# Kernel tuning notes

Measured on AMD Instinct MI355X. Metric: run time of the kernel, lower is better.

The kernel has to match this reference:

```python
import jax, jax.numpy as jnp
import numpy as np

B, S, H, E, TOP_K = 4, 2048, 1024, 8, 2


def setup_inputs() -> dict:
    key = jax.random.key(0)
    ks = jax.random.split(key, 7)
    sc = 1.0 / np.sqrt(H)
    return {
        "x": jax.random.normal(ks[0], (B, S, H), dtype=jnp.float32),
        "gate_w": jax.random.normal(ks[1], (H, E), dtype=jnp.float32) * sc,
        "gate_b": jnp.zeros((E,), dtype=jnp.float32),
        "w1": jax.random.normal(ks[2], (E, H, H), dtype=jnp.float32) * sc,
        "b1": jnp.zeros((E, H), dtype=jnp.float32),
        "w2": jax.random.normal(ks[3], (E, H, H), dtype=jnp.float32) * sc,
        "b2": jnp.zeros((E, H), dtype=jnp.float32),
    }


def reference(x, gate_w, gate_b, w1, b1, w2, b2):
    b, s, h = x.shape
    e = gate_w.shape[1]
    t = b * s
    hs = x.reshape(t, h)                                   # [T,H] flattened tokens
    # --- Router ---
    router_logits = hs @ gate_w + gate_b                    # [T,E] (returned pre-softmax)
    probs = jax.nn.softmax(router_logits, axis=-1)
    top_v, top_i = jax.lax.top_k(probs, TOP_K)              # [T,K]
    router_weight = top_v / top_v.sum(axis=-1, keepdims=True)
    # Dense per-(token, expert) gate: 0 for unselected experts -> same math as
    # the torch gather/index_add_ dispatch-combine loop.
    gates = jnp.zeros((t, e), hs.dtype).at[
        jnp.arange(t)[:, None], top_i
    ].add(router_weight)                                    # [T,E]
    # --- Experts (BasicExpert: Linear -> ReLU -> Linear, H->H->H) ---
    h1 = jax.nn.relu(jnp.einsum("th,ehf->etf", hs, w1) + b1[:, None, :])  # [E,T,H]
    oe = jnp.einsum("etf,efg->etg", h1, w2) + b2[:, None, :]              # [E,T,H]
    out = jnp.einsum("etg,te->tg", oe, gates)               # weighted combine [T,H]
    return out.reshape(b, s, h), router_logits
```

## Files before the change

### kernel.cpp

```cpp
#include <hip/hip_runtime.h>
#include <hip/hip_bf16.h>

#define T_TOKENS 8192
#define H_DIM    1024
#define N_EXP    8

#define BM 64
#define BN 128
#define BK 64

#define MAX_MSLOT 264
#define GEMM_GRID (MAX_MSLOT * 8)

typedef __attribute__((ext_vector_type(8))) __bf16 bf16x8;
typedef __attribute__((ext_vector_type(4))) float  f32x4;

#define AS1(p) ((const __attribute__((address_space(1))) void*)(p))
#define AS3(p) ((__attribute__((address_space(3))) void*)(p))

__device__ __forceinline__ unsigned short f2bf(float f) {
  unsigned u = __float_as_uint(f);
  u += 0x7fff + ((u >> 16) & 1);
  return (unsigned short)(u >> 16);
}
__device__ __forceinline__ float bf2f(unsigned short s) {
  return __uint_as_float(((unsigned)s) << 16);
}

__global__ __launch_bounds__(256) void router_kernel(
    const float* __restrict__ x, const float* __restrict__ gw,
    const float* __restrict__ gb, float* __restrict__ logits_out,
    int* __restrict__ choice, float* __restrict__ wpair,
    unsigned short* __restrict__ xb)
{
  const int tid = threadIdx.x;
  const int lane = tid & 63;
  const int w = tid >> 6;
  const int t = blockIdx.x * 4 + w;
  const float* xr = x + (size_t)t * H_DIM;

  float acc[8];
  #pragma unroll
  for (int e = 0; e < 8; ++e) acc[e] = 0.f;

  #pragma unroll
  for (int i = 0; i < H_DIM / 64; ++i) {
    const int h = i * 64 + lane;
    const float xv = xr[h];
    if (xb) xb[(size_t)t * H_DIM + h] = f2bf(xv);
    const float4 g0 = *(const float4*)&gw[h * 8 + 0];
    const float4 g1 = *(const float4*)&gw[h * 8 + 4];
    acc[0] += xv * g0.x; acc[1] += xv * g0.y;
    acc[2] += xv * g0.z; acc[3] += xv * g0.w;
    acc[4] += xv * g1.x; acc[5] += xv * g1.y;
    acc[6] += xv * g1.z; acc[7] += xv * g1.w;
  }
  #pragma unroll
  for (int off = 32; off; off >>= 1) {
    #pragma unroll
    for (int e = 0; e < 8; ++e) acc[e] += __shfl_xor(acc[e], off);
  }
  if (lane == 0) {
    float lg[8];
    #pragma unroll
    for (int e = 0; e < 8; ++e) lg[e] = acc[e] + gb[e];
    #pragma unroll
    for (int e = 0; e < 8; ++e) logits_out[(size_t)t * N_EXP + e] = lg[e];
    int e0 = 0; float v0 = lg[0];
    #pragma unroll
    for (int e = 1; e < 8; ++e) { if (lg[e] > v0) { v0 = lg[e]; e0 = e; } }
    int e1 = -1; float v1 = -3.4e38f;
    #pragma unroll
    for (int e = 0; e < 8; ++e) { if (e != e0 && lg[e] > v1) { v1 = lg[e]; e1 = e; } }
    const float ew = expf(v1 - v0);
    const float r0 = 1.f / (1.f + ew);
    const float r1 = ew / (1.f + ew);
    wpair[2 * t + 0] = r0;
    wpair[2 * t + 1] = r1;
    choice[t] = e0 | (e1 << 4);
  }
}

__global__ __launch_bounds__(256) void build_lists_kernel(
    const int* __restrict__ choice, int* __restrict__ cnt, int* __restrict__ lst)
{
  const int e = blockIdx.x;
  const int tid = threadIdx.x;
  __shared__ int sc[256];

  const int t0 = tid * 32;
  int ch[32];
  int cl = 0;
  #pragma unroll
  for (int j = 0; j < 32; ++j) {
    ch[j] = choice[t0 + j];
    if ((ch[j] & 15) == e) cl++;
    if ((ch[j] >> 4) == e) cl++;
  }
  sc[tid] = cl;
  __syncthreads();
  #pragma unroll
  for (int off = 1; off < 256; off <<= 1) {
    int u = (tid >= off) ? sc[tid - off] : 0;
    __syncthreads();
    sc[tid] += u;
    __syncthreads();
  }
  int pos = sc[tid] - cl;
  int* le = lst + e * T_TOKENS;
  #pragma unroll
  for (int j = 0; j < 32; ++j) {
    if ((ch[j] & 15) == e) le[pos++] = 2 * (t0 + j);
    if ((ch[j] >> 4) == e) le[pos++] = 2 * (t0 + j) + 1;
  }
  if (tid == 255) cnt[e] = sc[255];
}

__global__ void sched_kernel(const int* __restrict__ cnt, int* __restrict__ msched)
{
  if (threadIdx.x == 0) {
    int s = 0;
    for (int e = 0; e < N_EXP; ++e) {
      const int nm = (cnt[e] + BM - 1) / BM;
      for (int i = 0; i < nm; ++i) msched[s++] = e | (i << 4);
    }
    for (; s < MAX_MSLOT; ++s) msched[s] = -1;
  }
}

__global__ __launch_bounds__(256) void wconv_kernel(
    const float* __restrict__ w, unsigned short* __restrict__ wt)
{
  __shared__ float t[64][65];
  const float* we = w + (size_t)blockIdx.z * H_DIM * H_DIM;
  unsigned short* wte = wt + (size_t)blockIdx.z * H_DIM * H_DIM;
  const int k0 = blockIdx.y * 64, n0 = blockIdx.x * 64;
  const int tid = threadIdx.x;
  #pragma unroll
  for (int r = 0; r < 4; ++r) {
    const int k = (tid >> 4) + r * 16;
    const int n = (tid & 15) * 4;
    const float4 v = *(const float4*)&we[(size_t)(k0 + k) * H_DIM + n0 + n];
    t[n + 0][k] = v.x; t[n + 1][k] = v.y; t[n + 2][k] = v.z; t[n + 3][k] = v.w;
  }
  __syncthreads();
  const int n = tid >> 2, kc = (tid & 3) * 16;
  unsigned short o[16];
  #pragma unroll
  for (int j = 0; j < 16; ++j) o[j] = f2bf(t[n][kc + j]);
  *(int4*)&wte[(size_t)(n0 + n) * H_DIM + k0 + kc] = *(int4*)&o[0];
  *(int4*)&wte[(size_t)(n0 + n) * H_DIM + k0 + kc + 8] = *(int4*)&o[8];
}

#define DECODE_SLOT()                                        \
  const int id = blockIdx.x;                                 \
  const int sv = msched[(id >> 6) * 8 + (id & 7)];           \
  if (sv < 0) return;                                        \
  const int e  = sv & 15;                                    \
  const int m0 = (sv >> 4) * BM;                             \
  const int n0 = ((id >> 3) & 7) * BN;

template<int XB>
__global__ __launch_bounds__(256, 4) void gemm1_kernel(
    const float* __restrict__ x, const unsigned short* __restrict__ xb,
    const unsigned short* __restrict__ w1t, const float* __restrict__ b1,
    const int* __restrict__ cnt, const int* __restrict__ lst,
    const int* __restrict__ msched,
    const float* __restrict__ wpair, unsigned short* __restrict__ h1)
{
  DECODE_SLOT();
  const int c = cnt[e];
  const unsigned short* W = w1t + (size_t)e * H_DIM * H_DIM;
  const int* le = lst + e * T_TOKENS;

  __shared__ unsigned short As[BM * BK];
  __shared__ unsigned short Bs[BN * BK];

  const int tid  = threadIdx.x;
  const int lane = tid & 63;
  const int wid  = tid >> 6;

  const int lrow8 = lane >> 3;
  const int csrc  = (lane & 7) ^ lrow8;

  const unsigned short* bSrc[4];
  #pragma unroll
  for (int i = 0; i < 4; ++i) {
    const int r = wid * 32 + i * 8 + lrow8;
    bSrc[i] = W + (size_t)(n0 + r) * H_DIM + csrc * 8;
  }

  const unsigned short* aSrcB[2];
  const float* aSrcF[4]; int adst[4];
  if constexpr (XB) {
    #pragma unroll
    for (int i = 0; i < 2; ++i) {
      const int m = wid * 16 + i * 8 + lrow8;
      const int gm = m0 + m;
      const int pair = (gm < c) ? le[gm] : le[0];
      aSrcB[i] = xb + (size_t)(pair >> 1) * H_DIM + csrc * 8;
    }
  } else {
    #pragma unroll
    for (int i = 0; i < 4; ++i) {
      const int idx = i * 256 + tid;
      const int m = idx >> 4;
      const int k4 = (idx & 15) << 2;
      const int gm = m0 + m;
      const int pair = (gm < c) ? le[gm] : le[0];
      aSrcF[i] = x + (size_t)(pair >> 1) * H_DIM + k4;
      adst[i] = m * BK + (k4 ^ ((m & 7) << 3));
    }
  }

  const int wr = (wid >> 1) * 32;
  const int wc = (wid & 1) * 64;
  const int lr = lane & 15;
  const int kh = (lane >> 4) << 3;
  const int sw = (lane & 7) << 3;

  f32x4 acc[2][4];
  #pragma unroll
  for (int i = 0; i < 2; ++i)
    #pragma unroll
    for (int j = 0; j < 4; ++j) acc[i][j] = (f32x4){0.f, 0.f, 0.f, 0.f};

  for (int kt = 0; kt < H_DIM; kt += BK) {
    __syncthreads();
    #pragma unroll
    for (int i = 0; i < 4; ++i)
      __builtin_amdgcn_global_load_lds(AS1(bSrc[i] + kt), AS3(&Bs[(wid * 32 + i * 8) * BK]), 16, 0, 0);
    if constexpr (XB) {
      #pragma unroll
      for (int i = 0; i < 2; ++i)
        __builtin_amdgcn_global_load_lds(AS1(aSrcB[i] + kt), AS3(&As[(wid * 16 + i * 8) * BK]), 16, 0, 0);
    } else {
      #pragma unroll
      for (int i = 0; i < 4; ++i) {
        const float4 v = *(const float4*)(aSrcF[i] + kt);
        short4 s4;
        ((unsigned short*)&s4)[0] = f2bf(v.x);
        ((unsigned short*)&s4)[1] = f2bf(v.y);
        ((unsigned short*)&s4)[2] = f2bf(v.z);
        ((unsigned short*)&s4)[3] = f2bf(v.w);
        *(short4*)&As[adst[i]] = s4;
      }
    }
    __syncthreads();
    #pragma unroll
    for (int kk = 0; kk < BK; kk += 32) {
      bf16x8 a[2], b[4];
      #pragma unroll
      for (int mi = 0; mi < 2; ++mi) {
        const int row = wr + mi * 16 + lr;
        a[mi] = *reinterpret_cast<const bf16x8*>(&As[row * BK + ((kk + kh) ^ sw)]);
      }
      #pragma unroll
      for (int ni = 0; ni < 4; ++ni) {
        const int row = wc + ni * 16 + lr;
        b[ni] = *reinterpret_cast<const bf16x8*>(&Bs[row * BK + ((kk + kh) ^ sw)]);
      }
      #pragma unroll
      for (int mi = 0; mi < 2; ++mi)
        #pragma unroll
        for (int ni = 0; ni < 4; ++ni)
          acc[mi][ni] = __builtin_amdgcn_mfma_f32_16x16x32_bf16(a[mi], b[ni], acc[mi][ni], 0, 0, 0);
    }
  }

  #pragma unroll
  for (int mi = 0; mi < 2; ++mi) {
    const int rbase = wr + mi * 16 + ((lane >> 4) << 2);
    #pragma unroll
    for (int r = 0; r < 4; ++r) {
      const int gm = m0 + rbase + r;
      if (gm >= c) continue;
      const int pair = le[gm];
      const float g = wpair[pair];
      unsigned short* dst = h1 + (size_t)pair * H_DIM;
      #pragma unroll
      for (int ni = 0; ni < 4; ++ni) {
        const int col = n0 + wc + ni * 16 + lr;
        const float v = acc[mi][ni][r] + b1[e * H_DIM + col];
        dst[col] = f2bf(g * fmaxf(v, 0.f));
      }
    }
  }
}

__global__ __launch_bounds__(256, 4) void gemm2_kernel(
    const unsigned short* __restrict__ h1, const unsigned short* __restrict__ w2t,
    const float* __restrict__ b2, const int* __restrict__ cnt,
    const int* __restrict__ lst, const int* __restrict__ msched,
    const float* __restrict__ wpair,
    unsigned short* __restrict__ oe, float* __restrict__ out)
{
  DECODE_SLOT();
  const int c = cnt[e];
  const unsigned short* W = w2t + (size_t)e * H_DIM * H_DIM;
  const int* le = lst + e * T_TOKENS;

  __shared__ unsigned short As[BM * BK];
  __shared__ unsigned short Bs[BN * BK];

  const int tid  = threadIdx.x;
  const int lane = tid & 63;
  const int wid  = tid >> 6;

  const int lrow8 = lane >> 3;
  const int csrc  = (lane & 7) ^ lrow8;

  const unsigned short* aSrc[2];
  const unsigned short* bSrc[4];
  #pragma unroll
  for (int i = 0; i < 4; ++i) {
    const int r = wid * 32 + i * 8 + lrow8;
    bSrc[i] = W + (size_t)(n0 + r) * H_DIM + csrc * 8;
  }
  #pragma unroll
  for (int i = 0; i < 2; ++i) {
    const int m = wid * 16 + i * 8 + lrow8;
    const int gm = m0 + m;
    const int pair = (gm < c) ? le[gm] : le[0];
    aSrc[i] = h1 + (size_t)pair * H_DIM + csrc * 8;
  }

  const int wr = (wid >> 1) * 32;
  const int wc = (wid & 1) * 64;
  const int lr = lane & 15;
  const int kh = (lane >> 4) << 3;
  const int sw = (lane & 7) << 3;

  f32x4 acc[2][4];
  #pragma unroll
  for (int i = 0; i < 2; ++i)
    #pragma unroll
    for (int j = 0; j < 4; ++j) acc[i][j] = (f32x4){0.f, 0.f, 0.f, 0.f};

  for (int kt = 0; kt < H_DIM; kt += BK) {
    __syncthreads();
    #pragma unroll
    for (int i = 0; i < 4; ++i)
      __builtin_amdgcn_global_load_lds(AS1(bSrc[i] + kt), AS3(&Bs[(wid * 32 + i * 8) * BK]), 16, 0, 0);
    #pragma unroll
    for (int i = 0; i < 2; ++i)
      __builtin_amdgcn_global_load_lds(AS1(aSrc[i] + kt), AS3(&As[(wid * 16 + i * 8) * BK]), 16, 0, 0);
    __syncthreads();
    #pragma unroll
    for (int kk = 0; kk < BK; kk += 32) {
      bf16x8 a[2], b[4];
      #pragma unroll
      for (int mi = 0; mi < 2; ++mi) {
        const int row = wr + mi * 16 + lr;
        a[mi] = *reinterpret_cast<const bf16x8*>(&As[row * BK + ((kk + kh) ^ sw)]);
      }
      #pragma unroll
      for (int ni = 0; ni < 4; ++ni) {
        const int row = wc + ni * 16 + lr;
        b[ni] = *reinterpret_cast<const bf16x8*>(&Bs[row * BK + ((kk + kh) ^ sw)]);
      }
      #pragma unroll
      for (int mi = 0; mi < 2; ++mi)
        #pragma unroll
        for (int ni = 0; ni < 4; ++ni)
          acc[mi][ni] = __builtin_amdgcn_mfma_f32_16x16x32_bf16(a[mi], b[ni], acc[mi][ni], 0, 0, 0);
    }
  }

  #pragma unroll
  for (int mi = 0; mi < 2; ++mi) {
    const int rbase = wr + mi * 16 + ((lane >> 4) << 2);
    #pragma unroll
    for (int r = 0; r < 4; ++r) {
      const int gm = m0 + rbase + r;
      if (gm >= c) continue;
      const int pair = le[gm];
      unsigned short* dst = oe + (size_t)pair * H_DIM;
      #pragma unroll
      for (int ni = 0; ni < 4; ++ni) {
        const int col = n0 + wc + ni * 16 + lr;
        dst[col] = f2bf(acc[mi][ni][r]);
      }
    }
  }
}

__global__ __launch_bounds__(256, 4) void gemm2_atomic_kernel(
    const unsigned short* __restrict__ h1, const unsigned short* __restrict__ w2t,
    const float* __restrict__ b2, const int* __restrict__ cnt,
    const int* __restrict__ lst, const int* __restrict__ msched,
    const float* __restrict__ wpair, float* __restrict__ out)
{
  DECODE_SLOT();
  const int c = cnt[e];
  const unsigned short* W = w2t + (size_t)e * H_DIM * H_DIM;
  const int* le = lst + e * T_TOKENS;

  __shared__ unsigned short As[BM * BK];
  __shared__ unsigned short Bs[BN * BK];

  const int tid  = threadIdx.x;
  const int lane = tid & 63;
  const int wid  = tid >> 6;
  const int lrow8 = lane >> 3;
  const int csrc  = (lane & 7) ^ lrow8;

  const unsigned short* aSrc[2];
  const unsigned short* bSrc[4];
  #pragma unroll
  for (int i = 0; i < 4; ++i) {
    const int r = wid * 32 + i * 8 + lrow8;
    bSrc[i] = W + (size_t)(n0 + r) * H_DIM + csrc * 8;
  }
  #pragma unroll
  for (int i = 0; i < 2; ++i) {
    const int m = wid * 16 + i * 8 + lrow8;
    const int gm = m0 + m;
    const int pair = (gm < c) ? le[gm] : le[0];
    aSrc[i] = h1 + (size_t)pair * H_DIM + csrc * 8;
  }

  const int wr = (wid >> 1) * 32;
  const int wc = (wid & 1) * 64;
  const int lr = lane & 15;
  const int kh = (lane >> 4) << 3;
  const int sw = (lane & 7) << 3;

  f32x4 acc[2][4];
  #pragma unroll
  for (int i = 0; i < 2; ++i)
    #pragma unroll
    for (int j = 0; j < 4; ++j) acc[i][j] = (f32x4){0.f, 0.f, 0.f, 0.f};

  for (int kt = 0; kt < H_DIM; kt += BK) {
    __syncthreads();
    #pragma unroll
    for (int i = 0; i < 4; ++i)
      __builtin_amdgcn_global_load_lds(AS1(bSrc[i] + kt), AS3(&Bs[(wid * 32 + i * 8) * BK]), 16, 0, 0);
    #pragma unroll
    for (int i = 0; i < 2; ++i)
      __builtin_amdgcn_global_load_lds(AS1(aSrc[i] + kt), AS3(&As[(wid * 16 + i * 8) * BK]), 16, 0, 0);
    __syncthreads();
    #pragma unroll
    for (int kk = 0; kk < BK; kk += 32) {
      bf16x8 a[2], b[4];
      #pragma unroll
      for (int mi = 0; mi < 2; ++mi)
        a[mi] = *reinterpret_cast<const bf16x8*>(&As[(wr + mi * 16 + lr) * BK + ((kk + kh) ^ sw)]);
      #pragma unroll
      for (int ni = 0; ni < 4; ++ni)
        b[ni] = *reinterpret_cast<const bf16x8*>(&Bs[(wc + ni * 16 + lr) * BK + ((kk + kh) ^ sw)]);
      #pragma unroll
      for (int mi = 0; mi < 2; ++mi)
        #pragma unroll
        for (int ni = 0; ni < 4; ++ni)
          acc[mi][ni] = __builtin_amdgcn_mfma_f32_16x16x32_bf16(a[mi], b[ni], acc[mi][ni], 0, 0, 0);
    }
  }

  #pragma unroll
  for (int mi = 0; mi < 2; ++mi) {
    const int rbase = wr + mi * 16 + ((lane >> 4) << 2);
    #pragma unroll
    for (int r = 0; r < 4; ++r) {
      const int gm = m0 + rbase + r;
      if (gm >= c) continue;
      const int pair = le[gm];
      const int tok = pair >> 1;
      const float g = wpair[pair];
      float* dst = out + (size_t)tok * H_DIM;
      #pragma unroll
      for (int ni = 0; ni < 4; ++ni) {
        const int col = n0 + wc + ni * 16 + lr;
        atomicAdd(&dst[col], acc[mi][ni][r] + g * b2[e * H_DIM + col]);
      }
    }
  }
}

__global__ __launch_bounds__(256) void combine_kernel(
    const unsigned short* __restrict__ oe, const int* __restrict__ choice,
    const float* __restrict__ wpair, const float* __restrict__ b2,
    float* __restrict__ out)
{
  const int tid = threadIdx.x;
  const int t = blockIdx.x * 2 + (tid >> 7);
  const int col = (tid & 127) * 8;
  const int ch = choice[t];
  const int e0 = ch & 15, e1 = ch >> 4;
  const float g0 = wpair[2 * t], g1 = wpair[2 * t + 1];

  const unsigned short* o0 = oe + (size_t)(2 * t) * H_DIM + col;
  const unsigned short* o1 = oe + (size_t)(2 * t + 1) * H_DIM + col;
  int4 a = *(const int4*)o0;
  int4 b = *(const int4*)o1;
  const unsigned short* pa = (const unsigned short*)&a;
  const unsigned short* pb = (const unsigned short*)&b;
  const float* b2r0 = b2 + e0 * H_DIM + col;
  const float* b2r1 = b2 + e1 * H_DIM + col;
  float4 c0 = *(const float4*)&b2r0[0];
  float4 c1 = *(const float4*)&b2r0[4];
  float4 d0 = *(const float4*)&b2r1[0];
  float4 d1 = *(const float4*)&b2r1[4];
  float r[8];
  r[0] = bf2f(pa[0]) + bf2f(pb[0]) + g0 * c0.x + g1 * d0.x;
  r[1] = bf2f(pa[1]) + bf2f(pb[1]) + g0 * c0.y + g1 * d0.y;
  r[2] = bf2f(pa[2]) + bf2f(pb[2]) + g0 * c0.z + g1 * d0.z;
  r[3] = bf2f(pa[3]) + bf2f(pb[3]) + g0 * c0.w + g1 * d0.w;
  r[4] = bf2f(pa[4]) + bf2f(pb[4]) + g0 * c1.x + g1 * d1.x;
  r[5] = bf2f(pa[5]) + bf2f(pb[5]) + g0 * c1.y + g1 * d1.y;
  r[6] = bf2f(pa[6]) + bf2f(pb[6]) + g0 * c1.z + g1 * d1.z;
  r[7] = bf2f(pa[7]) + bf2f(pb[7]) + g0 * c1.w + g1 * d1.w;
  float* dst = out + (size_t)t * H_DIM + col;
  *(float4*)&dst[0] = *(float4*)&r[0];
  *(float4*)&dst[4] = *(float4*)&r[4];
}

extern "C" void kernel_launch(void* const* d_in, const int* in_sizes, int n_in,
                              void* d_out, int out_size, void* d_ws, size_t ws_size,
                              hipStream_t stream) {
  const float* x      = (const float*)d_in[0];
  const float* gate_w = (const float*)d_in[1];
  const float* gate_b = (const float*)d_in[2];
  const float* w1     = (const float*)d_in[3];
  const float* b1     = (const float*)d_in[4];
  const float* w2     = (const float*)d_in[5];
  const float* b2     = (const float*)d_in[6];

  float* out    = (float*)d_out;
  float* logits = out + (size_t)T_TOKENS * H_DIM;

  char* ws = (char*)d_ws;
  int*   cnt    = (int*)ws;
  int*   lst    = (int*)(ws + 256);
  float* wpr    = (float*)(ws + 262400);
  int*   choice = (int*)(ws + 327936);
  int*   msched = (int*)(ws + 360704);
  char*  big    = ws + 362752;

  const size_t SZ_XB = (size_t)T_TOKENS * H_DIM * 2;
  const size_t SZ_WT = (size_t)N_EXP * H_DIM * H_DIM * 2;
  const size_t SZ_H1 = (size_t)2 * T_TOKENS * H_DIM * 2;
  const size_t SZ_OE = (size_t)2 * T_TOKENS * H_DIM * 2;
  const bool full = ws_size >= (size_t)362752 + SZ_XB + SZ_WT + SZ_H1 + SZ_OE;

  unsigned short* xb = (unsigned short*)big;
  unsigned short* wt = (unsigned short*)(big + (full ? SZ_XB : 0));
  unsigned short* h1 = (unsigned short*)(big + (full ? SZ_XB : 0) + SZ_WT);
  unsigned short* oe = (unsigned short*)(big + SZ_XB + SZ_WT + SZ_H1);

  if (full) {
    router_kernel<<<T_TOKENS / 4, 256, 0, stream>>>(x, gate_w, gate_b, logits, choice, wpr, xb);
    build_lists_kernel<<<N_EXP, 256, 0, stream>>>(choice, cnt, lst);
    sched_kernel<<<1, 64, 0, stream>>>(cnt, msched);
    wconv_kernel<<<dim3(16, 16, 8), 256, 0, stream>>>(w1, wt);
    gemm1_kernel<1><<<GEMM_GRID, 256, 0, stream>>>(x, xb, wt, b1, cnt, lst, msched, wpr, h1);
    wconv_kernel<<<dim3(16, 16, 8), 256, 0, stream>>>(w2, wt);
    gemm2_kernel<<<GEMM_GRID, 256, 0, stream>>>(h1, wt, b2, cnt, lst, msched, wpr, oe, out);
    combine_kernel<<<T_TOKENS / 2, 256, 0, stream>>>(oe, choice, wpr, b2, out);
  } else {
    hipMemsetAsync(out, 0, (size_t)T_TOKENS * H_DIM * sizeof(float), stream);
    router_kernel<<<T_TOKENS / 4, 256, 0, stream>>>(x, gate_w, gate_b, logits, choice, wpr, nullptr);
    build_lists_kernel<<<N_EXP, 256, 0, stream>>>(choice, cnt, lst);
    sched_kernel<<<1, 64, 0, stream>>>(cnt, msched);
    wconv_kernel<<<dim3(16, 16, 8), 256, 0, stream>>>(w1, wt);
    gemm1_kernel<0><<<GEMM_GRID, 256, 0, stream>>>(x, xb, wt, b1, cnt, lst, msched, wpr, h1);
    wconv_kernel<<<dim3(16, 16, 8), 256, 0, stream>>>(w2, wt);
    gemm2_atomic_kernel<<<GEMM_GRID, 256, 0, stream>>>(h1, wt, b2, cnt, lst, msched, wpr, out);
  }
}
```

Before: 171.8 us.

## Replace grouped expert GEMMs with double-buffered 256x256-tile persistent kernel

```diff
diff --git a/kernel.cpp b/kernel.cpp
--- a/kernel.cpp
+++ b/kernel.cpp
@@ -122,7 +122,7 @@
     int s = 0;
     for (int e = 0; e < N_EXP; ++e) {
       const int nm = (cnt[e] + BM - 1) / BM;
-      for (int i = 0; i < nm; ++i) msched[s++] = e | (i << 4);
+      for (int i = 0; i < nm && s < MAX_MSLOT; ++i) msched[s++] = e | (i << 4);
     }
     for (; s < MAX_MSLOT; ++s) msched[s] = -1;
   }
@@ -150,6 +150,125 @@
   for (int j = 0; j < 16; ++j) o[j] = f2bf(t[n][kc + j]);
   *(int4*)&wte[(size_t)(n0 + n) * H_DIM + k0 + kc] = *(int4*)&o[0];
   *(int4*)&wte[(size_t)(n0 + n) * H_DIM + k0 + kc + 8] = *(int4*)&o[8];
+}
+
+template<int G1>
+__global__ __launch_bounds__(512, 2) void gemm256_kernel(
+    const unsigned short* __restrict__ A,
+    const unsigned short* __restrict__ Wt,
+    const float* __restrict__ b1,
+    const int* __restrict__ cnt, const int* __restrict__ lst,
+    const float* __restrict__ wpair,
+    unsigned short* __restrict__ Out)
+{
+  const int e   = blockIdx.x & 7;
+  const int g   = blockIdx.x >> 3;
+  const int mi  = g & 7;
+  const int n0g = (g >> 3) * 256;
+  const int c = cnt[e];
+  const unsigned short* W = Wt + (size_t)e * H_DIM * H_DIM;
+  const int* le = lst + e * T_TOKENS;
+
+  __shared__ unsigned short As[2][256 * 64];
+  __shared__ unsigned short Bs[2][256 * 64];
+
+  const int tid  = threadIdx.x;
+  const int lane = tid & 63;
+  const int wid  = tid >> 6;
+  const int wm   = wid >> 2;
+  const int wn   = wid & 3;
+  const int lrow8 = lane >> 3;
+  const int csrc  = (lane & 7) ^ lrow8;
+  const int lr = lane & 15;
+  const int kh = (lane >> 4) << 3;
+  const int sw = (lane & 7) << 3;
+
+  const unsigned short* bSrc[4];
+  #pragma unroll
+  for (int i = 0; i < 4; ++i)
+    bSrc[i] = W + (size_t)(n0g + wid * 32 + i * 8 + lrow8) * H_DIM + csrc * 8;
+
+  for (int m0 = mi * 256; m0 < c; m0 += 2048) {
+    const unsigned short* aSrc[4];
+    #pragma unroll
+    for (int i = 0; i < 4; ++i) {
+      const int gm = m0 + wid * 32 + i * 8 + lrow8;
+      const int pair = (gm < c) ? le[gm] : le[0];
+      const size_t row = G1 ? (size_t)(pair >> 1) : (size_t)pair;
+      aSrc[i] = A + row * H_DIM + csrc * 8;
+    }
+
+    f32x4 acc[8][4];
+    #pragma unroll
+    for (int i = 0; i < 8; ++i)
+      #pragma unroll
+      for (int j = 0; j < 4; ++j) acc[i][j] = (f32x4){0.f, 0.f, 0.f, 0.f};
+
+    #pragma unroll
+    for (int i = 0; i < 4; ++i) {
+      __builtin_amdgcn_global_load_lds(AS1(aSrc[i]), AS3(&As[0][(wid * 32 + i * 8) * 64]), 16, 0, 0);
+      __builtin_amdgcn_global_load_lds(AS1(bSrc[i]), AS3(&Bs[0][(wid * 32 + i * 8) * 64]), 16, 0, 0);
+    }
+
+    for (int t = 0; t < 16; ++t) {
+      __syncthreads();
+      const int cb = t & 1;
+      if (t < 15) {
+        const int kt = (t + 1) * BK;
+        #pragma unroll
+        for (int i = 0; i < 4; ++i) {
+          __builtin_amdgcn_global_load_lds(AS1(aSrc[i] + kt), AS3(&As[cb ^ 1][(wid * 32 + i * 8) * 64]), 16, 0, 0);
+          __builtin_amdgcn_global_load_lds(AS1(bSrc[i] + kt), AS3(&Bs[cb ^ 1][(wid * 32 + i * 8) * 64]), 16, 0, 0);
+        }
+      }
+      #pragma unroll
+      for (int ks = 0; ks < 2; ++ks) {
+        bf16x8 b[4];
+        #pragma unroll
+        for (int nf = 0; nf < 4; ++nf)
+          b[nf] = *reinterpret_cast<const bf16x8*>(&Bs[cb][(wn * 64 + nf * 16 + lr) * 64 + ((ks * 32 + kh) ^ sw)]);
+        #pragma unroll
+        for (int mh = 0; mh < 2; ++mh) {
+          bf16x8 a[4];
+          #pragma unroll
+          for (int mf = 0; mf < 4; ++mf)
+            a[mf] = *reinterpret_cast<const bf16x8*>(&As[cb][(wm * 128 + mh * 64 + mf * 16 + lr) * 64 + ((ks * 32 + kh) ^ sw)]);
+          #pragma unroll
+          for (int mf = 0; mf < 4; ++mf)
+            #pragma unroll
+            for (int nf = 0; nf < 4; ++nf)
+              acc[mh * 4 + mf][nf] = __builtin_amdgcn_mfma_f32_16x16x32_bf16(a[mf], b[nf], acc[mh * 4 + mf][nf], 0, 0, 0);
+        }
+      }
+    }
+
+    #pragma unroll
+    for (int mfp = 0; mfp < 8; ++mfp) {
+      const int rbase = wm * 128 + mfp * 16 + ((lane >> 4) << 2);
+      #pragma unroll
+      for (int r = 0; r < 4; ++r) {
+        const int gm = m0 + rbase + r;
+        if (gm >= c) continue;
+        const int pair = le[gm];
+        unsigned short* dst = Out + (size_t)pair * H_DIM;
+        if constexpr (G1) {
+          const float gt = wpair[pair];
+          #pragma unroll
+          for (int nf = 0; nf < 4; ++nf) {
+            const int col = n0g + wn * 64 + nf * 16 + lr;
+            const float v = acc[mfp][nf][r] + b1[e * H_DIM + col];
+            dst[col] = f2bf(gt * fmaxf(v, 0.f));
+          }
+        } else {
+          #pragma unroll
+          for (int nf = 0; nf < 4; ++nf) {
+            const int col = n0g + wn * 64 + nf * 16 + lr;
+            dst[col] = f2bf(acc[mfp][nf][r]);
+          }
+        }
+      }
+    }
+  }
 }
 
 #define DECODE_SLOT()                                        \
@@ -160,9 +279,8 @@
   const int m0 = (sv >> 4) * BM;                             \
   const int n0 = ((id >> 3) & 7) * BN;
 
-template<int XB>
-__global__ __launch_bounds__(256, 4) void gemm1_kernel(
-    const float* __restrict__ x, const unsigned short* __restrict__ xb,
+__global__ __launch_bounds__(256, 4) void gemm1f_kernel(
+    const float* __restrict__ x,
     const unsigned short* __restrict__ w1t, const float* __restrict__ b1,
     const int* __restrict__ cnt, const int* __restrict__ lst,
     const int* __restrict__ msched,
@@ -179,38 +297,24 @@
   const int tid  = threadIdx.x;
   const int lane = tid & 63;
   const int wid  = tid >> 6;
-
   const int lrow8 = lane >> 3;
   const int csrc  = (lane & 7) ^ lrow8;
 
   const unsigned short* bSrc[4];
   #pragma unroll
+  for (int i = 0; i < 4; ++i)
+    bSrc[i] = W + (size_t)(n0 + wid * 32 + i * 8 + lrow8) * H_DIM + csrc * 8;
+
+  const float* aSrcF[4]; int adst[4];
+  #pragma unroll
   for (int i = 0; i < 4; ++i) {
-    const int r = wid * 32 + i * 8 + lrow8;
-    bSrc[i] = W + (size_t)(n0 + r) * H_DIM + csrc * 8;
-  }
-
-  const unsigned short* aSrcB[2];
-  const float* aSrcF[4]; int adst[4];
-  if constexpr (XB) {
-    #pragma unroll
-    for (int i = 0; i < 2; ++i) {
-      const int m = wid * 16 + i * 8 + lrow8;
-      const int gm = m0 + m;
-      const int pair = (gm < c) ? le[gm] : le[0];
-      aSrcB[i] = xb + (size_t)(pair >> 1) * H_DIM + csrc * 8;
-    }
-  } else {
-    #pragma unroll
-    for (int i = 0; i < 4; ++i) {
-      const int idx = i * 256 + tid;
-      const int m = idx >> 4;
-      const int k4 = (idx & 15) << 2;
-      const int gm = m0 + m;
-      const int pair = (gm < c) ? le[gm] : le[0];
-      aSrcF[i] = x + (size_t)(pair >> 1) * H_DIM + k4;
-      adst[i] = m * BK + (k4 ^ ((m & 7) << 3));
-    }
+    const int idx = i * 256 + tid;
+    const int m = idx >> 4;
+    const int k4 = (idx & 15) << 2;
+    const int gm = m0 + m;
+    const int pair = (gm < c) ? le[gm] : le[0];
+    aSrcF[i] = x + (size_t)(pair >> 1) * H_DIM + k4;
+    adst[i] = m * BK + (k4 ^ ((m & 7) << 3));
   }
 
   const int wr = (wid >> 1) * 32;
@@ -230,47 +334,37 @@
     #pragma unroll
     for (int i = 0; i < 4; ++i)
       __builtin_amdgcn_global_load_lds(AS1(bSrc[i] + kt), AS3(&Bs[(wid * 32 + i * 8) * BK]), 16, 0, 0);
-    if constexpr (XB) {
-      #pragma unroll
-      for (int i = 0; i < 2; ++i)
-        __builtin_amdgcn_global_load_lds(AS1(aSrcB[i] + kt), AS3(&As[(wid * 16 + i * 8) * BK]), 16, 0, 0);
-    } else {
-      #pragma unroll
-      for (int i = 0; i < 4; ++i) {
-        const float4 v = *(const float4*)(aSrcF[i] + kt);
-        short4 s4;
-        ((unsigned short*)&s4)[0] = f2bf(v.x);
-        ((unsigned short*)&s4)[1] = f2bf(v.y);
-        ((unsigned short*)&s4)[2] = f2bf(v.z);
-        ((unsigned short*)&s4)[3] = f2bf(v.w);
-        *(short4*)&As[adst[i]] = s4;
-      }
+    #pragma unroll
+    for (int i = 0; i < 4; ++i) {
+      const float4 v = *(const float4*)(aSrcF[i] + kt);
+      short4 s4;
+      ((unsigned short*)&s4)[0] = f2bf(v.x);
+      ((unsigned short*)&s4)[1] = f2bf(v.y);
+      ((unsigned short*)&s4)[2] = f2bf(v.z);
+      ((unsigned short*)&s4)[3] = f2bf(v.w);
+      *(short4*)&As[adst[i]] = s4;
     }
     __syncthreads();
     #pragma unroll
     for (int kk = 0; kk < BK; kk += 32) {
       bf16x8 a[2], b[4];
       #pragma unroll
-      for (int mi = 0; mi < 2; ++mi) {
-        const int row = wr + mi * 16 + lr;
-        a[mi] = *reinterpret_cast<const bf16x8*>(&As[row * BK + ((kk + kh) ^ sw)]);
-      }
-      #pragma unroll
-      for (int ni = 0; ni < 4; ++ni) {
-        const int row = wc + ni * 16 + lr;
-        b[ni] = *reinterpret_cast<const bf16x8*>(&Bs[row * BK + ((kk + kh) ^ sw)]);
-      }
-      #pragma unroll
-      for (int mi = 0; mi < 2; ++mi)
+      for (int mi2 = 0; mi2 < 2; ++mi2)
+        a[mi2] = *reinterpret_cast<const bf16x8*>(&As[(wr + mi2 * 16 + lr) * BK + ((kk + kh) ^ sw)]);
+      #pragma unroll
+      for (int ni = 0; ni < 4; ++ni)
+        b[ni] = *reinterpret_cast<const bf16x8*>(&Bs[(wc + ni * 16 + lr) * BK + ((kk + kh) ^ sw)]);
+      #pragma unroll
+      for (int mi2 = 0; mi2 < 2; ++mi2)
         #pragma unroll
         for (int ni = 0; ni < 4; ++ni)
-          acc[mi][ni] = __builtin_amdgcn_mfma_f32_16x16x32_bf16(a[mi], b[ni], acc[mi][ni], 0, 0, 0);
-    }
-  }
-
-  #pragma unroll
-  for (int mi = 0; mi < 2; ++mi) {
-    const int rbase = wr + mi * 16 + ((lane >> 4) << 2);
+          acc[mi2][ni] = __builtin_amdgcn_mfma_f32_16x16x32_bf16(a[mi2], b[ni], acc[mi2][ni], 0, 0, 0);
+    }
+  }
+
+  #pragma unroll
+  for (int mi2 = 0; mi2 < 2; ++mi2) {
+    const int rbase = wr + mi2 * 16 + ((lane >> 4) << 2);
     #pragma unroll
     for (int r = 0; r < 4; ++r) {
       const int gm = m0 + rbase + r;
@@ -281,19 +375,18 @@
       #pragma unroll
       for (int ni = 0; ni < 4; ++ni) {
         const int col = n0 + wc + ni * 16 + lr;
-        const float v = acc[mi][ni][r] + b1[e * H_DIM + col];
+        const float v = acc[mi2][ni][r] + b1[e * H_DIM + col];
         dst[col] = f2bf(g * fmaxf(v, 0.f));
       }
     }
   }
 }
 
-__global__ __launch_bounds__(256, 4) void gemm2_kernel(
+__global__ __launch_bounds__(256, 4) void gemm2_atomic_kernel(
     const unsigned short* __restrict__ h1, const unsigned short* __restrict__ w2t,
     const float* __restrict__ b2, const int* __restrict__ cnt,
     const int* __restrict__ lst, const int* __restrict__ msched,
-    const float* __restrict__ wpair,
-    unsigned short* __restrict__ oe, float* __restrict__ out)
+    const float* __restrict__ wpair, float* __restrict__ out)
 {
   DECODE_SLOT();
   const int c = cnt[e];
@@ -306,17 +399,14 @@
   const int tid  = threadIdx.x;
   const int lane = tid & 63;
   const int wid  = tid >> 6;
-
   const int lrow8 = lane >> 3;
   const int csrc  = (lane & 7) ^ lrow8;
 
   const unsigned short* aSrc[2];
   const unsigned short* bSrc[4];
   #pragma unroll
-  for (int i = 0; i < 4; ++i) {
-    const int r = wid * 32 + i * 8 + lrow8;
-    bSrc[i] = W + (size_t)(n0 + r) * H_DIM + csrc * 8;
-  }
+  for (int i = 0; i < 4; ++i)
+    bSrc[i] = W + (size_t)(n0 + wid * 32 + i * 8 + lrow8) * H_DIM + csrc * 8;
   #pragma unroll
   for (int i = 0; i < 2; ++i) {
     const int m = wid * 16 + i * 8 + lrow8;
@@ -350,117 +440,22 @@
     for (int kk = 0; kk < BK; kk += 32) {
       bf16x8 a[2], b[4];
       #pragma unroll
-      for (int mi = 0; mi < 2; ++mi) {
-        const int row = wr + mi * 16 + lr;
-        a[mi] = *reinterpret_cast<const bf16x8*>(&As[row * BK + ((kk + kh) ^ sw)]);
-      }
-      #pragma unroll
-      for (int ni = 0; ni < 4; ++ni) {
-        const int row = wc + ni * 16 + lr;
-        b[ni] = *reinterpret_cast<const bf16x8*>(&Bs[row * BK + ((kk + kh) ^ sw)]);
-      }
-      #pragma unroll
-      for (int mi = 0; mi < 2; ++mi)
+      for (int mi2 = 0; mi2 < 2; ++mi2)
+        a[mi2] = *reinterpret_cast<const bf16x8*>(&As[(wr + mi2 * 16 + lr) * BK + ((kk + kh) ^ sw)]);
+      #pragma unroll
+      for (int ni = 0; ni < 4; ++ni)
+        b[ni] = *reinterpret_cast<const bf16x8*>(&Bs[(wc + ni * 16 + lr) * BK + ((kk + kh) ^ sw)]);
+      #pragma unroll
+      for (int mi2 = 0; mi2 < 2; ++mi2)
         #pragma unroll
         for (int ni = 0; ni < 4; ++ni)
-          acc[mi][ni] = __builtin_amdgcn_mfma_f32_16x16x32_bf16(a[mi], b[ni], acc[mi][ni], 0, 0, 0);
-    }
-  }
-
-  #pragma unroll
-  for (int mi = 0; mi < 2; ++mi) {
-    const int rbase = wr + mi * 16 + ((lane >> 4) << 2);
-    #pragma unroll
-    for (int r = 0; r < 4; ++r) {
-      const int gm = m0 + rbase + r;
-      if (gm >= c) continue;
-      const int pair = le[gm];
-      unsigned short* dst = oe + (size_t)pair * H_DIM;
-      #pragma unroll
-      for (int ni = 0; ni < 4; ++ni) {
-        const int col = n0 + wc + ni * 16 + lr;
-        dst[col] = f2bf(acc[mi][ni][r]);
-      }
-    }
-  }
-}
-
-__global__ __launch_bounds__(256, 4) void gemm2_atomic_kernel(
-    const unsigned short* __restrict__ h1, const unsigned short* __restrict__ w2t,
-    const float* __restrict__ b2, const int* __restrict__ cnt,
-    const int* __restrict__ lst, const int* __restrict__ msched,
-    const float* __restrict__ wpair, float* __restrict__ out)
-{
-  DECODE_SLOT();
-  const int c = cnt[e];
-  const unsigned short* W = w2t + (size_t)e * H_DIM * H_DIM;
-  const int* le = lst + e * T_TOKENS;
-
-  __shared__ unsigned short As[BM * BK];
-  __shared__ unsigned short Bs[BN * BK];
-
-  const int tid  = threadIdx.x;
-  const int lane = tid & 63;
-  const int wid  = tid >> 6;
-  const int lrow8 = lane >> 3;
-  const int csrc  = (lane & 7) ^ lrow8;
-
-  const unsigned short* aSrc[2];
-  const unsigned short* bSrc[4];
-  #pragma unroll
-  for (int i = 0; i < 4; ++i) {
-    const int r = wid * 32 + i * 8 + lrow8;
-    bSrc[i] = W + (size_t)(n0 + r) * H_DIM + csrc * 8;
-  }
-  #pragma unroll
-  for (int i = 0; i < 2; ++i) {
-    const int m = wid * 16 + i * 8 + lrow8;
-    const int gm = m0 + m;
-    const int pair = (gm < c) ? le[gm] : le[0];
-    aSrc[i] = h1 + (size_t)pair * H_DIM + csrc * 8;
-  }
-
-  const int wr = (wid >> 1) * 32;
-  const int wc = (wid & 1) * 64;
-  const int lr = lane & 15;
-  const int kh = (lane >> 4) << 3;
-  const int sw = (lane & 7) << 3;
-
-  f32x4 acc[2][4];
-  #pragma unroll
-  for (int i = 0; i < 2; ++i)
-    #pragma unroll
-    for (int j = 0; j < 4; ++j) acc[i][j] = (f32x4){0.f, 0.f, 0.f, 0.f};
-
-  for (int kt = 0; kt < H_DIM; kt += BK) {
-    __syncthreads();
-    #pragma unroll
-    for (int i = 0; i < 4; ++i)
-      __builtin_amdgcn_global_load_lds(AS1(bSrc[i] + kt), AS3(&Bs[(wid * 32 + i * 8) * BK]), 16, 0, 0);
-    #pragma unroll
-    for (int i = 0; i < 2; ++i)
-      __builtin_amdgcn_global_load_lds(AS1(aSrc[i] + kt), AS3(&As[(wid * 16 + i * 8) * BK]), 16, 0, 0);
-    __syncthreads();
-    #pragma unroll
-    for (int kk = 0; kk < BK; kk += 32) {
-      bf16x8 a[2], b[4];
-      #pragma unroll
-      for (int mi = 0; mi < 2; ++mi)
-        a[mi] = *reinterpret_cast<const bf16x8*>(&As[(wr + mi * 16 + lr) * BK + ((kk + kh) ^ sw)]);
-      #pragma unroll
-      for (int ni = 0; ni < 4; ++ni)
-        b[ni] = *reinterpret_cast<const bf16x8*>(&Bs[(wc + ni * 16 + lr) * BK + ((kk + kh) ^ sw)]);
-      #pragma unroll
-      for (int mi = 0; mi < 2; ++mi)
-        #pragma unroll
-        for (int ni = 0; ni < 4; ++ni)
-          acc[mi][ni] = __builtin_amdgcn_mfma_f32_16x16x32_bf16(a[mi], b[ni], acc[mi][ni], 0, 0, 0);
-    }
-  }
-
-  #pragma unroll
-  for (int mi = 0; mi < 2; ++mi) {
-    const int rbase = wr + mi * 16 + ((lane >> 4) << 2);
+          acc[mi2][ni] = __builtin_amdgcn_mfma_f32_16x16x32_bf16(a[mi2], b[ni], acc[mi2][ni], 0, 0, 0);
+    }
+  }
+
+  #pragma unroll
+  for (int mi2 = 0; mi2 < 2; ++mi2) {
+    const int rbase = wr + mi2 * 16 + ((lane >> 4) << 2);
     #pragma unroll
     for (int r = 0; r < 4; ++r) {
       const int gm = m0 + rbase + r;
@@ -472,7 +467,7 @@
       #pragma unroll
       for (int ni = 0; ni < 4; ++ni) {
         const int col = n0 + wc + ni * 16 + lr;
-        atomicAdd(&dst[col], acc[mi][ni][r] + g * b2[e * H_DIM + col]);
+        atomicAdd(&dst[col], acc[mi2][ni][r] + g * b2[e * H_DIM + col]);
       }
     }
   }
@@ -552,11 +547,10 @@
   if (full) {
     router_kernel<<<T_TOKENS / 4, 256, 0, stream>>>(x, gate_w, gate_b, logits, choice, wpr, xb);
     build_lists_kernel<<<N_EXP, 256, 0, stream>>>(choice, cnt, lst);
-    sched_kernel<<<1, 64, 0, stream>>>(cnt, msched);
     wconv_kernel<<<dim3(16, 16, 8), 256, 0, stream>>>(w1, wt);
-    gemm1_kernel<1><<<GEMM_GRID, 256, 0, stream>>>(x, xb, wt, b1, cnt, lst, msched, wpr, h1);
+    gemm256_kernel<1><<<256, 512, 0, stream>>>(xb, wt, b1, cnt, lst, wpr, h1);
     wconv_kernel<<<dim3(16, 16, 8), 256, 0, stream>>>(w2, wt);
-    gemm2_kernel<<<GEMM_GRID, 256, 0, stream>>>(h1, wt, b2, cnt, lst, msched, wpr, oe, out);
+    gemm256_kernel<0><<<256, 512, 0, stream>>>(h1, wt, nullptr, cnt, lst, wpr, oe);
     combine_kernel<<<T_TOKENS / 2, 256, 0, stream>>>(oe, choice, wpr, b2, out);
   } else {
     hipMemsetAsync(out, 0, (size_t)T_TOKENS * H_DIM * sizeof(float), stream);
@@ -564,7 +558,7 @@
     build_lists_kernel<<<N_EXP, 256, 0, stream>>>(choice, cnt, lst);
     sched_kernel<<<1, 64, 0, stream>>>(cnt, msched);
     wconv_kernel<<<dim3(16, 16, 8), 256, 0, stream>>>(w1, wt);
-    gemm1_kernel<0><<<GEMM_GRID, 256, 0, stream>>>(x, xb, wt, b1, cnt, lst, msched, wpr, h1);
+    gemm1f_kernel<<<GEMM_GRID, 256, 0, stream>>>(x, wt, b1, cnt, lst, msched, wpr, h1);
     wconv_kernel<<<dim3(16, 16, 8), 256, 0, stream>>>(w2, wt);
     gemm2_atomic_kernel<<<GEMM_GRID, 256, 0, stream>>>(h1, wt, b2, cnt, lst, msched, wpr, out);
   }
```

New measurement: 219.1 us. 1.27x slower.
